# Kernel optimization log

Measured on AMD Instinct MI355X. Metric: run time of the kernel, lower is better.

## Reference

```python
import jax, jax.numpy as jnp
import numpy as np

B = 8192          # number of bags/users
L = 50            # items per bag (uniform)
NNZ = B * L
VOCAB = 100000
D = 64            # embedding_dim
ATT = 64          # att_dim
K = 4             # acc_user_num


def setup_inputs() -> dict:
    key = jax.random.key(0)
    k1, k2, k3, k4, k5 = jax.random.split(key, 5)
    # flat CSR indices, sorted within each row (module assumes coalesced order)
    idx = jax.random.randint(k1, (B, L), 0, VOCAB, dtype=jnp.int64)
    input_ = jnp.sort(idx, axis=1).reshape(NNZ)
    offsets = (jnp.arange(B, dtype=jnp.int64) * L)
    emb_weight = jax.random.normal(k2, (VOCAB, D), dtype=jnp.float32) * 0.05
    proj_w = jax.random.normal(k3, (ATT, D), dtype=jnp.float32) * (1.0 / np.sqrt(D))
    proj_b = jax.random.normal(k4, (ATT,), dtype=jnp.float32) * 0.01
    att_h = jax.random.truncated_normal(k5, -2.0, 2.0, (ATT, K), dtype=jnp.float32) * 0.01
    return {"input_": input_, "offsets": offsets, "emb_weight": emb_weight,
            "proj_w": proj_w, "proj_b": proj_b, "att_h": att_h}


def reference(input_, offsets, emb_weight, proj_w, proj_b, att_h):
    nnz = input_.shape[0]
    nseg = offsets.shape[0]
    # segment id for each flat element (offsets are sorted row starts)
    seg = jnp.searchsorted(offsets, jnp.arange(nnz), side="right") - 1  # [nnz]
    att_emb = emb_weight[input_]                                        # [nnz, D]
    att = jnp.tanh(att_emb @ proj_w.T + proj_b) @ att_h                 # [nnz, K]
    # ragged per-segment softmax over each attention column
    m = jax.ops.segment_max(att, seg, num_segments=nseg)                # [B, K]
    e = jnp.exp(att - m[seg])
    s = jax.ops.segment_sum(e, seg, num_segments=nseg)                  # [B, K]
    smax = e / s[seg]                                                   # [nnz, K]
    # weighted segment-sum pooling -> [B, K, D]
    weighted = smax[:, :, None] * att_emb[:, None, :]                   # [nnz, K, D]
    result = jax.ops.segment_sum(weighted, seg, num_segments=nseg)
    return result
```

## Files before the change

kernel.cpp:

```cpp
#include <hip/hip_runtime.h>
#include <hip/hip_bf16.h>

typedef __attribute__((ext_vector_type(4))) float  f32x4;
typedef __attribute__((ext_vector_type(4))) short  s16x4;
typedef __attribute__((ext_vector_type(8))) short  s16x8;

#define SH 72

__device__ inline short f2bf(float x) {
    return __builtin_bit_cast(short, __float2bfloat16(x));
}
__device__ inline s16x8 pack8(f32x4 a, f32x4 b) {
    s16x8 r;
    r[0] = f2bf(a[0]); r[1] = f2bf(a[1]); r[2] = f2bf(a[2]); r[3] = f2bf(a[3]);
    r[4] = f2bf(b[0]); r[5] = f2bf(b[1]); r[6] = f2bf(b[2]); r[7] = f2bf(b[3]);
    return r;
}

__global__ __launch_bounds__(256) void conv_kernel(
    const float* __restrict__ emb, short* __restrict__ emb_bf, int n8)
{
    int t = blockIdx.x * 256 + threadIdx.x;
    int stride = gridDim.x * 256;
    for (int i = t; i < n8; i += stride) {
        f32x4 a = *(const f32x4*)(emb + (size_t)i * 8);
        f32x4 b = *(const f32x4*)(emb + (size_t)i * 8 + 4);
        *(s16x8*)(emb_bf + (size_t)i * 8) = pack8(a, b);
    }
}

__global__ __launch_bounds__(256, 4) void pooled_attn_kernel(
    const int*   __restrict__ input_,
    const int*   __restrict__ offsets,
    const short* __restrict__ emb_bf,
    const float* __restrict__ pw,
    const float* __restrict__ pb,
    const float* __restrict__ ah,
    float*       __restrict__ out,
    int B, int nnz)
{
    __shared__ __align__(16) char  s_ovl[16384];
    __shared__ __align__(16) float s_bias[64];
    __shared__ __align__(16) short s_h_all[4][16 * SH];
    __shared__ __align__(16) short s_amat[4][1024];

    const int tid  = threadIdx.x;
    const int lane = tid & 63;
    const int wv   = tid >> 6;
    const int col  = lane & 15;
    const int quad = lane >> 4;

    short* s_pw  = (short*)s_ovl;
    short* s_ahp = (short*)(s_ovl + 9216);
    short* sh    = s_h_all[wv];
    short* am    = s_amat[wv];
    short* poolw = (short*)(s_ovl + wv * 4096);

    {
        int r = tid >> 2, seg = tid & 3;
        const float* rp = pw + r * 64 + seg * 16;
        f32x4 a0 = *(const f32x4*)(rp);
        f32x4 a1 = *(const f32x4*)(rp + 4);
        f32x4 a2 = *(const f32x4*)(rp + 8);
        f32x4 a3 = *(const f32x4*)(rp + 12);
        *(s16x8*)(s_pw + r * SH + seg * 16)     = pack8(a0, a1);
        *(s16x8*)(s_pw + r * SH + seg * 16 + 8) = pack8(a2, a3);
    }
    if (tid < 128) {
        int c = tid >> 6, l = tid & 63;
        int q = l >> 4, cc = l & 15;
        s16x8 v;
        #pragma unroll
        for (int j = 0; j < 8; ++j) {
            int a = c * 32 + q * 8 + j;
            v[j] = (cc < 4) ? f2bf(ah[a * 4 + cc]) : (short)0;
        }
        *(s16x8*)(s_ahp + (c * 64 + l) * 8) = v;
    }
    if (tid < 64) s_bias[tid] = pb[tid];
    __syncthreads();

    const s16x8 ahA0 = *(const s16x8*)(s_ahp + lane * 8);
    const s16x8 ahA1 = *(const s16x8*)(s_ahp + (64 + lane) * 8);
    s16x8 pwA[4][2];
    #pragma unroll
    for (int mt = 0; mt < 4; ++mt) {
        pwA[mt][0] = *(const s16x8*)(s_pw + (mt * 16 + col) * SH + quad * 8);
        pwA[mt][1] = *(const s16x8*)(s_pw + (mt * 16 + col) * SH + 32 + quad * 8);
    }
    __syncthreads();

    const int bag = blockIdx.x * 4 + wv;
    if (bag >= B) return;
    const int start = offsets[bag];
    const int end   = (bag + 1 < B) ? offsets[bag + 1] : nnz;
    int n = end - start;
    if (n > 64) n = 64;
    float* op = out + (size_t)bag * 256 + lane;
    if (n < 1) {
        op[0] = 0.f; op[64] = 0.f; op[128] = 0.f; op[192] = 0.f;
        return;
    }
    const int idx_l = input_[start + (lane < n ? lane : n - 1)];

    {
        s16x8 z = {0, 0, 0, 0, 0, 0, 0, 0};
        *(s16x8*)(am + lane * 16)     = z;
        *(s16x8*)(am + lane * 16 + 8) = z;
    }

    s16x8 gB0[4], gB1[4];
    #pragma unroll
    for (int nt = 0; nt < 4; ++nt) {
        int row = __shfl(idx_l, nt * 16 + col);
        const short* rp = emb_bf + (size_t)(unsigned)row * 64 + quad * 8;
        gB0[nt] = *(const s16x8*)(rp);
        gB1[nt] = *(const s16x8*)(rp + 32);
    }

    f32x4 p0 = {0,0,0,0}, p1 = {0,0,0,0}, p2 = {0,0,0,0}, p3 = {0,0,0,0};
    f32x4 ssum = {0, 0, 0, 0};

    #pragma unroll
    for (int nt = 0; nt < 4; ++nt) {
        {
            int i  = ((nt & 1) << 4) + col;
            int wb = ((((i >> 3) ^ quad) & 3) << 3) + (i & 7);
            #pragma unroll
            for (int j = 0; j < 8; ++j) {
                poolw[(quad * 8 + j) * 32 + wb]        = gB0[nt][j];
                poolw[(quad * 8 + j) * 32 + 1024 + wb] = gB1[nt][j];
            }
        }

        #pragma unroll
        for (int mt = 0; mt < 4; ++mt) {
            f32x4 acc = *(const f32x4*)(s_bias + mt * 16 + quad * 4);
            acc = __builtin_amdgcn_mfma_f32_16x16x32_bf16(pwA[mt][0], gB0[nt], acc, 0, 0, 0);
            acc = __builtin_amdgcn_mfma_f32_16x16x32_bf16(pwA[mt][1], gB1[nt], acc, 0, 0, 0);
            s16x4 hp;
            #pragma unroll
            for (int r = 0; r < 4; ++r) {
                float z = acc[r];
                float t2 = z * z;
                float h = z * (1.f + t2 * (-0.33333334f +
                               t2 * (0.13333333f + t2 * (-0.05396825f))));
                hp[r] = f2bf(h);
            }
            *(s16x4*)(sh + col * SH + mt * 16 + quad * 4) = hp;
        }
        f32x4 a2 = {0.f, 0.f, 0.f, 0.f};
        s16x8 b20 = *(const s16x8*)(sh + col * SH + quad * 8);
        s16x8 b21 = *(const s16x8*)(sh + col * SH + 32 + quad * 8);
        a2 = __builtin_amdgcn_mfma_f32_16x16x32_bf16(ahA0, b20, a2, 0, 0, 0);
        a2 = __builtin_amdgcn_mfma_f32_16x16x32_bf16(ahA1, b21, a2, 0, 0, 0);

        const bool pad = (nt * 16 + col >= n);
        f32x4 ev;
        #pragma unroll
        for (int k = 0; k < 4; ++k) {
            float e = __expf(a2[k]);
            e = pad ? 0.f : e;
            ev[k] = e;
            ssum[k] += (quad == 0) ? e : 0.f;
        }
        if (quad == 0) {
            int item = nt * 16 + col;
            #pragma unroll
            for (int r = 0; r < 4; ++r)
                am[(r * 64 + item) ^ (r << 3)] = f2bf(ev[r]);
        }

        if ((nt & 1) == 1) {
            const int s  = nt >> 1;
            const int c3 = col >> 3;
            int sa = (col * 64 + (s << 5) + (quad << 3)) ^ ((col & 7) << 3);
            s16x8 af = *(const s16x8*)(am + sa);
            s16x8 b0 = *(const s16x8*)(poolw + (0 * 16 + col) * 32 + (((quad ^ (0 + c3)) & 3) << 3));
            s16x8 b1 = *(const s16x8*)(poolw + (1 * 16 + col) * 32 + (((quad ^ (2 + c3)) & 3) << 3));
            s16x8 b2 = *(const s16x8*)(poolw + (2 * 16 + col) * 32 + (((quad ^ (4 + c3)) & 3) << 3));
            s16x8 b3 = *(const s16x8*)(poolw + (3 * 16 + col) * 32 + (((quad ^ (6 + c3)) & 3) << 3));
            p0 = __builtin_amdgcn_mfma_f32_16x16x32_bf16(af, b0, p0, 0, 0, 0);
            p1 = __builtin_amdgcn_mfma_f32_16x16x32_bf16(af, b1, p1, 0, 0, 0);
            p2 = __builtin_amdgcn_mfma_f32_16x16x32_bf16(af, b2, p2, 0, 0, 0);
            p3 = __builtin_amdgcn_mfma_f32_16x16x32_bf16(af, b3, p3, 0, 0, 0);
        }
    }

    #pragma unroll
    for (int m = 1; m <= 32; m <<= 1)
        #pragma unroll
        for (int k = 0; k < 4; ++k)
            ssum[k] += __shfl_xor(ssum[k], m, 64);
    f32x4 rs;
    #pragma unroll
    for (int k = 0; k < 4; ++k)
        rs[k] = __builtin_amdgcn_rcpf(ssum[k]);

    asm volatile("" ::: "memory");
    float* om = (float*)am;
    if (quad == 0) {
        { int d =      col; int sl = (d & 56) | ((d + (d >> 3)) & 7); *(f32x4*)(om + sl * 4) = p0; }
        { int d = 16 + col; int sl = (d & 56) | ((d + (d >> 3)) & 7); *(f32x4*)(om + sl * 4) = p1; }
        { int d = 32 + col; int sl = (d & 56) | ((d + (d >> 3)) & 7); *(f32x4*)(om + sl * 4) = p2; }
        { int d = 48 + col; int sl = (d & 56) | ((d + (d >> 3)) & 7); *(f32x4*)(om + sl * 4) = p3; }
    }
    int sl = (lane & 56) | ((lane + (lane >> 3)) & 7);
    f32x4 po = *(const f32x4*)(om + sl * 4);
    op[0]   = po[0] * rs[0];
    op[64]  = po[1] * rs[1];
    op[128] = po[2] * rs[2];
    op[192] = po[3] * rs[3];
}

extern "C" void kernel_launch(void* const* d_in, const int* in_sizes, int n_in,
                              void* d_out, int out_size, void* d_ws, size_t ws_size,
                              hipStream_t stream) {
    const int*   input_  = (const int*)d_in[0];
    const int*   offsets = (const int*)d_in[1];
    const float* emb     = (const float*)d_in[2];
    const float* pw      = (const float*)d_in[3];
    const float* pb      = (const float*)d_in[4];
    const float* ah      = (const float*)d_in[5];
    float* out = (float*)d_out;
    const int nnz   = in_sizes[0];
    const int B     = in_sizes[1];
    const int vocab_elems = in_sizes[2];

    short* emb_bf = (short*)d_ws;

    conv_kernel<<<1024, 256, 0, stream>>>(emb, emb_bf, vocab_elems / 8);
    pooled_attn_kernel<<<(B + 3) / 4, 256, 0, stream>>>(input_, offsets, emb_bf,
                                                        pw, pb, ah, out, B, nnz);
}
```

Measured before the change: 105.6 us.

## Drop the bf16 table pre-conversion; gather fp32 rows and convert in-register

The separate kernel that converted the entire 100k×64 fp32 embedding table to bf16 is removed. The main kernel now gathers fp32 rows directly and packs them to bf16 in registers, so it no longer reads and writes the whole table each call and only touches the ~410k gathered rows at double the byte width. It also moves the bias into registers and drops the padded h tile in favour of an XOR-swizzled 64-wide layout. It raises the occupancy hint to 5 and shortens the tanh polynomial by one term, which slightly reduces accuracy.

After: 178.3 us. +68.8%, slower.

```diff
diff --git a/kernel.cpp b/kernel.cpp
--- a/kernel.cpp
+++ b/kernel.cpp
@@ -4,8 +4,6 @@
 typedef __attribute__((ext_vector_type(4))) float  f32x4;
 typedef __attribute__((ext_vector_type(4))) short  s16x4;
 typedef __attribute__((ext_vector_type(8))) short  s16x8;
-
-#define SH 72
 
 __device__ inline short f2bf(float x) {
     return __builtin_bit_cast(short, __float2bfloat16(x));
@@ -17,22 +15,10 @@
     return r;
 }
 
-__global__ __launch_bounds__(256) void conv_kernel(
-    const float* __restrict__ emb, short* __restrict__ emb_bf, int n8)
-{
-    int t = blockIdx.x * 256 + threadIdx.x;
-    int stride = gridDim.x * 256;
-    for (int i = t; i < n8; i += stride) {
-        f32x4 a = *(const f32x4*)(emb + (size_t)i * 8);
-        f32x4 b = *(const f32x4*)(emb + (size_t)i * 8 + 4);
-        *(s16x8*)(emb_bf + (size_t)i * 8) = pack8(a, b);
-    }
-}
-
-__global__ __launch_bounds__(256, 4) void pooled_attn_kernel(
+__global__ __launch_bounds__(256, 5) void pooled_attn_kernel(
     const int*   __restrict__ input_,
     const int*   __restrict__ offsets,
-    const short* __restrict__ emb_bf,
+    const float* __restrict__ emb,
     const float* __restrict__ pw,
     const float* __restrict__ pb,
     const float* __restrict__ ah,
@@ -40,8 +26,7 @@
     int B, int nnz)
 {
     __shared__ __align__(16) char  s_ovl[16384];
-    __shared__ __align__(16) float s_bias[64];
-    __shared__ __align__(16) short s_h_all[4][16 * SH];
+    __shared__ __align__(16) short s_h_all[4][16 * 64];
     __shared__ __align__(16) short s_amat[4][1024];
 
     const int tid  = threadIdx.x;
@@ -49,6 +34,7 @@
     const int wv   = tid >> 6;
     const int col  = lane & 15;
     const int quad = lane >> 4;
+    const int xm   = (col & 7) << 3;
 
     short* s_pw  = (short*)s_ovl;
     short* s_ahp = (short*)(s_ovl + 9216);
@@ -63,8 +49,8 @@
         f32x4 a1 = *(const f32x4*)(rp + 4);
         f32x4 a2 = *(const f32x4*)(rp + 8);
         f32x4 a3 = *(const f32x4*)(rp + 12);
-        *(s16x8*)(s_pw + r * SH + seg * 16)     = pack8(a0, a1);
-        *(s16x8*)(s_pw + r * SH + seg * 16 + 8) = pack8(a2, a3);
+        *(s16x8*)(s_pw + r * 72 + seg * 16)     = pack8(a0, a1);
+        *(s16x8*)(s_pw + r * 72 + seg * 16 + 8) = pack8(a2, a3);
     }
     if (tid < 128) {
         int c = tid >> 6, l = tid & 63;
@@ -77,7 +63,6 @@
         }
         *(s16x8*)(s_ahp + (c * 64 + l) * 8) = v;
     }
-    if (tid < 64) s_bias[tid] = pb[tid];
     __syncthreads();
 
     const s16x8 ahA0 = *(const s16x8*)(s_ahp + lane * 8);
@@ -85,8 +70,8 @@
     s16x8 pwA[4][2];
     #pragma unroll
     for (int mt = 0; mt < 4; ++mt) {
-        pwA[mt][0] = *(const s16x8*)(s_pw + (mt * 16 + col) * SH + quad * 8);
-        pwA[mt][1] = *(const s16x8*)(s_pw + (mt * 16 + col) * SH + 32 + quad * 8);
+        pwA[mt][0] = *(const s16x8*)(s_pw + (mt * 16 + col) * 72 + quad * 8);
+        pwA[mt][1] = *(const s16x8*)(s_pw + (mt * 16 + col) * 72 + 32 + quad * 8);
     }
     __syncthreads();
 
@@ -103,6 +88,11 @@
     }
     const int idx_l = input_[start + (lane < n ? lane : n - 1)];
 
+    f32x4 biasv[4];
+    #pragma unroll
+    for (int mt = 0; mt < 4; ++mt)
+        biasv[mt] = *(const f32x4*)(pb + mt * 16 + quad * 4);
+
     {
         s16x8 z = {0, 0, 0, 0, 0, 0, 0, 0};
         *(s16x8*)(am + lane * 16)     = z;
@@ -113,9 +103,13 @@
     #pragma unroll
     for (int nt = 0; nt < 4; ++nt) {
         int row = __shfl(idx_l, nt * 16 + col);
-        const short* rp = emb_bf + (size_t)(unsigned)row * 64 + quad * 8;
-        gB0[nt] = *(const s16x8*)(rp);
-        gB1[nt] = *(const s16x8*)(rp + 32);
+        const float* rp = emb + (size_t)(unsigned)row * 64 + quad * 8;
+        f32x4 a0 = *(const f32x4*)(rp);
+        f32x4 a1 = *(const f32x4*)(rp + 4);
+        f32x4 b0 = *(const f32x4*)(rp + 32);
+        f32x4 b1 = *(const f32x4*)(rp + 36);
+        gB0[nt] = pack8(a0, a1);
+        gB1[nt] = pack8(b0, b1);
     }
 
     f32x4 p0 = {0,0,0,0}, p1 = {0,0,0,0}, p2 = {0,0,0,0}, p3 = {0,0,0,0};
@@ -135,7 +129,7 @@
 
         #pragma unroll
         for (int mt = 0; mt < 4; ++mt) {
-            f32x4 acc = *(const f32x4*)(s_bias + mt * 16 + quad * 4);
+            f32x4 acc = biasv[mt];
             acc = __builtin_amdgcn_mfma_f32_16x16x32_bf16(pwA[mt][0], gB0[nt], acc, 0, 0, 0);
             acc = __builtin_amdgcn_mfma_f32_16x16x32_bf16(pwA[mt][1], gB1[nt], acc, 0, 0, 0);
             s16x4 hp;
@@ -143,15 +137,14 @@
             for (int r = 0; r < 4; ++r) {
                 float z = acc[r];
                 float t2 = z * z;
-                float h = z * (1.f + t2 * (-0.33333334f +
-                               t2 * (0.13333333f + t2 * (-0.05396825f))));
+                float h = z * (1.f + t2 * (-0.33333334f + t2 * 0.13333334f));
                 hp[r] = f2bf(h);
             }
-            *(s16x4*)(sh + col * SH + mt * 16 + quad * 4) = hp;
+            *(s16x4*)(sh + col * 64 + ((mt * 16 + quad * 4) ^ xm)) = hp;
         }
         f32x4 a2 = {0.f, 0.f, 0.f, 0.f};
-        s16x8 b20 = *(const s16x8*)(sh + col * SH + quad * 8);
-        s16x8 b21 = *(const s16x8*)(sh + col * SH + 32 + quad * 8);
+        s16x8 b20 = *(const s16x8*)(sh + col * 64 + ((quad * 8) ^ xm));
+        s16x8 b21 = *(const s16x8*)(sh + col * 64 + ((32 + quad * 8) ^ xm));
         a2 = __builtin_amdgcn_mfma_f32_16x16x32_bf16(ahA0, b20, a2, 0, 0, 0);
         a2 = __builtin_amdgcn_mfma_f32_16x16x32_bf16(ahA1, b21, a2, 0, 0, 0);
 
@@ -223,13 +216,10 @@
     const float* pb      = (const float*)d_in[4];
     const float* ah      = (const float*)d_in[5];
     float* out = (float*)d_out;
-    const int nnz   = in_sizes[0];
-    const int B     = in_sizes[1];
-    const int vocab_elems = in_sizes[2];
-
-    short* emb_bf = (short*)d_ws;
-
-    conv_kernel<<<1024, 256, 0, stream>>>(emb, emb_bf, vocab_elems / 8);
-    pooled_attn_kernel<<<(B + 3) / 4, 256, 0, stream>>>(input_, offsets, emb_bf,
+    const int nnz = in_sizes[0];
+    const int B   = in_sizes[1];
+    (void)d_ws; (void)ws_size;
+
+    pooled_attn_kernel<<<(B + 3) / 4, 256, 0, stream>>>(input_, offsets, emb,
                                                         pw, pb, ah, out, B, nnz);
 }
```

## Process two bags per wave with prefetch of second bag's embedding rows

Applied to the files above, without the earlier changes.

Each wave now handles two bags (grid halved). The second bag's embedding gathers are issued after the first bag's compute loop, so they overlap its softmax reduction and output stage, and the one-time per-block setup of weights in LDS and registers is amortized over twice as many bags. It costs extra registers for the prefetch buffers and leaves fewer blocks to hide latency across the GPU.

Result: slower. 108.5 us (+2.7%).

```diff
diff --git a/kernel.cpp b/kernel.cpp
--- a/kernel.cpp
+++ b/kernel.cpp
@@ -27,6 +27,130 @@
         f32x4 b = *(const f32x4*)(emb + (size_t)i * 8 + 4);
         *(s16x8*)(emb_bf + (size_t)i * 8) = pack8(a, b);
     }
+}
+
+
+template<bool PF>
+__device__ __attribute__((always_inline)) inline void process_bag(
+    int n, int pf_idx, const short* __restrict__ emb_bf,
+    const s16x8 (&pwA)[4][2], const s16x8& ahA0, const s16x8& ahA1,
+    const float* s_bias, short* sh, short* am, short* poolw,
+    float* op, int col, int quad,
+    s16x8 (&g0)[4], s16x8 (&g1)[4],
+    s16x8 (&pf0)[4], s16x8 (&pf1)[4])
+{
+    {
+        const int lane = quad * 16 + col;
+        s16x8 z = {0, 0, 0, 0, 0, 0, 0, 0};
+        *(s16x8*)(am + lane * 16)     = z;
+        *(s16x8*)(am + lane * 16 + 8) = z;
+    }
+
+    f32x4 p0 = {0,0,0,0}, p1 = {0,0,0,0}, p2 = {0,0,0,0}, p3 = {0,0,0,0};
+    f32x4 ssum = {0, 0, 0, 0};
+
+    #pragma unroll
+    for (int nt = 0; nt < 4; ++nt) {
+        {
+            int i  = ((nt & 1) << 4) + col;
+            int wb = ((((i >> 3) ^ quad) & 3) << 3) + (i & 7);
+            #pragma unroll
+            for (int j = 0; j < 8; ++j) {
+                poolw[(quad * 8 + j) * 32 + wb]        = g0[nt][j];
+                poolw[(quad * 8 + j) * 32 + 1024 + wb] = g1[nt][j];
+            }
+        }
+
+        #pragma unroll
+        for (int mt = 0; mt < 4; ++mt) {
+            f32x4 acc = *(const f32x4*)(s_bias + mt * 16 + quad * 4);
+            acc = __builtin_amdgcn_mfma_f32_16x16x32_bf16(pwA[mt][0], g0[nt], acc, 0, 0, 0);
+            acc = __builtin_amdgcn_mfma_f32_16x16x32_bf16(pwA[mt][1], g1[nt], acc, 0, 0, 0);
+            s16x4 hp;
+            #pragma unroll
+            for (int r = 0; r < 4; ++r) {
+                float z = acc[r];
+                float t2 = z * z;
+                float h = z * (1.f + t2 * (-0.33333334f +
+                               t2 * (0.13333333f + t2 * (-0.05396825f))));
+                hp[r] = f2bf(h);
+            }
+            *(s16x4*)(sh + col * SH + mt * 16 + quad * 4) = hp;
+        }
+        f32x4 a2 = {0.f, 0.f, 0.f, 0.f};
+        s16x8 b20 = *(const s16x8*)(sh + col * SH + quad * 8);
+        s16x8 b21 = *(const s16x8*)(sh + col * SH + 32 + quad * 8);
+        a2 = __builtin_amdgcn_mfma_f32_16x16x32_bf16(ahA0, b20, a2, 0, 0, 0);
+        a2 = __builtin_amdgcn_mfma_f32_16x16x32_bf16(ahA1, b21, a2, 0, 0, 0);
+
+        const bool pad = (nt * 16 + col >= n);
+        f32x4 ev;
+        #pragma unroll
+        for (int k = 0; k < 4; ++k) {
+            float e = __expf(a2[k]);
+            e = pad ? 0.f : e;
+            ev[k] = e;
+            ssum[k] += (quad == 0) ? e : 0.f;
+        }
+        if (quad == 0) {
+            int item = nt * 16 + col;
+            #pragma unroll
+            for (int r = 0; r < 4; ++r)
+                am[(r * 64 + item) ^ (r << 3)] = f2bf(ev[r]);
+        }
+
+        if ((nt & 1) == 1) {
+            const int s  = nt >> 1;
+            const int c3 = col >> 3;
+            int sa = (col * 64 + (s << 5) + (quad << 3)) ^ ((col & 7) << 3);
+            s16x8 af = *(const s16x8*)(am + sa);
+            s16x8 b0 = *(const s16x8*)(poolw + (0 * 16 + col) * 32 + (((quad ^ (0 + c3)) & 3) << 3));
+            s16x8 b1 = *(const s16x8*)(poolw + (1 * 16 + col) * 32 + (((quad ^ (2 + c3)) & 3) << 3));
+            s16x8 b2 = *(const s16x8*)(poolw + (2 * 16 + col) * 32 + (((quad ^ (4 + c3)) & 3) << 3));
+            s16x8 b3 = *(const s16x8*)(poolw + (3 * 16 + col) * 32 + (((quad ^ (6 + c3)) & 3) << 3));
+            p0 = __builtin_amdgcn_mfma_f32_16x16x32_bf16(af, b0, p0, 0, 0, 0);
+            p1 = __builtin_amdgcn_mfma_f32_16x16x32_bf16(af, b1, p1, 0, 0, 0);
+            p2 = __builtin_amdgcn_mfma_f32_16x16x32_bf16(af, b2, p2, 0, 0, 0);
+            p3 = __builtin_amdgcn_mfma_f32_16x16x32_bf16(af, b3, p3, 0, 0, 0);
+        }
+    }
+
+    if (PF) {
+        #pragma unroll
+        for (int nt = 0; nt < 4; ++nt) {
+            int row = __shfl(pf_idx, nt * 16 + col);
+            const short* rp = emb_bf + (size_t)(unsigned)row * 64 + quad * 8;
+            pf0[nt] = *(const s16x8*)(rp);
+            pf1[nt] = *(const s16x8*)(rp + 32);
+        }
+    }
+
+    #pragma unroll
+    for (int m = 1; m <= 32; m <<= 1)
+        #pragma unroll
+        for (int k = 0; k < 4; ++k)
+            ssum[k] += __shfl_xor(ssum[k], m, 64);
+    f32x4 rs;
+    #pragma unroll
+    for (int k = 0; k < 4; ++k)
+        rs[k] = __builtin_amdgcn_rcpf(ssum[k]);
+
+    asm volatile("" ::: "memory");
+    float* om = (float*)am;
+    if (quad == 0) {
+        { int d =      col; int sl = (d & 56) | ((d + (d >> 3)) & 7); *(f32x4*)(om + sl * 4) = p0; }
+        { int d = 16 + col; int sl = (d & 56) | ((d + (d >> 3)) & 7); *(f32x4*)(om + sl * 4) = p1; }
+        { int d = 32 + col; int sl = (d & 56) | ((d + (d >> 3)) & 7); *(f32x4*)(om + sl * 4) = p2; }
+        { int d = 48 + col; int sl = (d & 56) | ((d + (d >> 3)) & 7); *(f32x4*)(om + sl * 4) = p3; }
+    }
+    const int lane = quad * 16 + col;
+    int sl = (lane & 56) | ((lane + (lane >> 3)) & 7);
+    f32x4 po = *(const f32x4*)(om + sl * 4);
+    asm volatile("" ::: "memory");
+    op[0]   = po[0] * rs[0];
+    op[64]  = po[1] * rs[1];
+    op[128] = po[2] * rs[2];
+    op[192] = po[3] * rs[3];
 }
 
 __global__ __launch_bounds__(256, 4) void pooled_attn_kernel(
@@ -90,127 +214,60 @@
     }
     __syncthreads();
 
-    const int bag = blockIdx.x * 4 + wv;
-    if (bag >= B) return;
-    const int start = offsets[bag];
-    const int end   = (bag + 1 < B) ? offsets[bag + 1] : nnz;
-    int n = end - start;
-    if (n > 64) n = 64;
-    float* op = out + (size_t)bag * 256 + lane;
-    if (n < 1) {
-        op[0] = 0.f; op[64] = 0.f; op[128] = 0.f; op[192] = 0.f;
-        return;
-    }
-    const int idx_l = input_[start + (lane < n ? lane : n - 1)];
-
-    {
-        s16x8 z = {0, 0, 0, 0, 0, 0, 0, 0};
-        *(s16x8*)(am + lane * 16)     = z;
-        *(s16x8*)(am + lane * 16 + 8) = z;
-    }
-
-    s16x8 gB0[4], gB1[4];
+    const int bagA = blockIdx.x * 8 + wv;
+    const int bagB = bagA + 4;
+
+    int nA = 0, nB = 0, idxA = 0, idxB = 0;
+    if (bagA < B) {
+        int s = offsets[bagA];
+        int e = (bagA + 1 < B) ? offsets[bagA + 1] : nnz;
+        nA = e - s; if (nA > 64) nA = 64;
+        if (nA >= 1) idxA = input_[s + (lane < nA ? lane : nA - 1)];
+    }
+    if (bagB < B) {
+        int s = offsets[bagB];
+        int e = (bagB + 1 < B) ? offsets[bagB + 1] : nnz;
+        nB = e - s; if (nB > 64) nB = 64;
+        if (nB >= 1) idxB = input_[s + (lane < nB ? lane : nB - 1)];
+    }
+
+    s16x8 gA0[4], gA1[4], gB0[4], gB1[4];
     #pragma unroll
     for (int nt = 0; nt < 4; ++nt) {
-        int row = __shfl(idx_l, nt * 16 + col);
+        int row = __shfl(idxA, nt * 16 + col);
         const short* rp = emb_bf + (size_t)(unsigned)row * 64 + quad * 8;
-        gB0[nt] = *(const s16x8*)(rp);
-        gB1[nt] = *(const s16x8*)(rp + 32);
-    }
-
-    f32x4 p0 = {0,0,0,0}, p1 = {0,0,0,0}, p2 = {0,0,0,0}, p3 = {0,0,0,0};
-    f32x4 ssum = {0, 0, 0, 0};
-
-    #pragma unroll
-    for (int nt = 0; nt < 4; ++nt) {
-        {
-            int i  = ((nt & 1) << 4) + col;
-            int wb = ((((i >> 3) ^ quad) & 3) << 3) + (i & 7);
-            #pragma unroll
-            for (int j = 0; j < 8; ++j) {
-                poolw[(quad * 8 + j) * 32 + wb]        = gB0[nt][j];
-                poolw[(quad * 8 + j) * 32 + 1024 + wb] = gB1[nt][j];
+        gA0[nt] = *(const s16x8*)(rp);
+        gA1[nt] = *(const s16x8*)(rp + 32);
+    }
+
+    if (bagA < B) {
+        float* opA = out + (size_t)bagA * 256 + lane;
+        if (nA >= 1) {
+            process_bag<true>(nA, idxB, emb_bf, pwA, ahA0, ahA1,
+                              s_bias, sh, am, poolw, opA, col, quad,
+                              gA0, gA1, gB0, gB1);
+        } else {
+            opA[0] = 0.f; opA[64] = 0.f; opA[128] = 0.f; opA[192] = 0.f;
+            #pragma unroll
+            for (int nt = 0; nt < 4; ++nt) {
+                int row = __shfl(idxB, nt * 16 + col);
+                const short* rp = emb_bf + (size_t)(unsigned)row * 64 + quad * 8;
+                gB0[nt] = *(const s16x8*)(rp);
+                gB1[nt] = *(const s16x8*)(rp + 32);
             }
         }
-
-        #pragma unroll
-        for (int mt = 0; mt < 4; ++mt) {
-            f32x4 acc = *(const f32x4*)(s_bias + mt * 16 + quad * 4);
-            acc = __builtin_amdgcn_mfma_f32_16x16x32_bf16(pwA[mt][0], gB0[nt], acc, 0, 0, 0);
-            acc = __builtin_amdgcn_mfma_f32_16x16x32_bf16(pwA[mt][1], gB1[nt], acc, 0, 0, 0);
-            s16x4 hp;
-            #pragma unroll
-            for (int r = 0; r < 4; ++r) {
-                float z = acc[r];
-                float t2 = z * z;
-                float h = z * (1.f + t2 * (-0.33333334f +
-                               t2 * (0.13333333f + t2 * (-0.05396825f))));
-                hp[r] = f2bf(h);
-            }
-            *(s16x4*)(sh + col * SH + mt * 16 + quad * 4) = hp;
-        }
-        f32x4 a2 = {0.f, 0.f, 0.f, 0.f};
-        s16x8 b20 = *(const s16x8*)(sh + col * SH + quad * 8);
-        s16x8 b21 = *(const s16x8*)(sh + col * SH + 32 + quad * 8);
-        a2 = __builtin_amdgcn_mfma_f32_16x16x32_bf16(ahA0, b20, a2, 0, 0, 0);
-        a2 = __builtin_amdgcn_mfma_f32_16x16x32_bf16(ahA1, b21, a2, 0, 0, 0);
-
-        const bool pad = (nt * 16 + col >= n);
-        f32x4 ev;
-        #pragma unroll
-        for (int k = 0; k < 4; ++k) {
-            float e = __expf(a2[k]);
-            e = pad ? 0.f : e;
-            ev[k] = e;
-            ssum[k] += (quad == 0) ? e : 0.f;
-        }
-        if (quad == 0) {
-            int item = nt * 16 + col;
-            #pragma unroll
-            for (int r = 0; r < 4; ++r)
-                am[(r * 64 + item) ^ (r << 3)] = f2bf(ev[r]);
-        }
-
-        if ((nt & 1) == 1) {
-            const int s  = nt >> 1;
-            const int c3 = col >> 3;
-            int sa = (col * 64 + (s << 5) + (quad << 3)) ^ ((col & 7) << 3);
-            s16x8 af = *(const s16x8*)(am + sa);
-            s16x8 b0 = *(const s16x8*)(poolw + (0 * 16 + col) * 32 + (((quad ^ (0 + c3)) & 3) << 3));
-            s16x8 b1 = *(const s16x8*)(poolw + (1 * 16 + col) * 32 + (((quad ^ (2 + c3)) & 3) << 3));
-            s16x8 b2 = *(const s16x8*)(poolw + (2 * 16 + col) * 32 + (((quad ^ (4 + c3)) & 3) << 3));
-            s16x8 b3 = *(const s16x8*)(poolw + (3 * 16 + col) * 32 + (((quad ^ (6 + c3)) & 3) << 3));
-            p0 = __builtin_amdgcn_mfma_f32_16x16x32_bf16(af, b0, p0, 0, 0, 0);
-            p1 = __builtin_amdgcn_mfma_f32_16x16x32_bf16(af, b1, p1, 0, 0, 0);
-            p2 = __builtin_amdgcn_mfma_f32_16x16x32_bf16(af, b2, p2, 0, 0, 0);
-            p3 = __builtin_amdgcn_mfma_f32_16x16x32_bf16(af, b3, p3, 0, 0, 0);
-        }
-    }
-
-    #pragma unroll
-    for (int m = 1; m <= 32; m <<= 1)
-        #pragma unroll
-        for (int k = 0; k < 4; ++k)
-            ssum[k] += __shfl_xor(ssum[k], m, 64);
-    f32x4 rs;
-    #pragma unroll
-    for (int k = 0; k < 4; ++k)
-        rs[k] = __builtin_amdgcn_rcpf(ssum[k]);
-
-    asm volatile("" ::: "memory");
-    float* om = (float*)am;
-    if (quad == 0) {
-        { int d =      col; int sl = (d & 56) | ((d + (d >> 3)) & 7); *(f32x4*)(om + sl * 4) = p0; }
-        { int d = 16 + col; int sl = (d & 56) | ((d + (d >> 3)) & 7); *(f32x4*)(om + sl * 4) = p1; }
-        { int d = 32 + col; int sl = (d & 56) | ((d + (d >> 3)) & 7); *(f32x4*)(om + sl * 4) = p2; }
-        { int d = 48 + col; int sl = (d & 56) | ((d + (d >> 3)) & 7); *(f32x4*)(om + sl * 4) = p3; }
-    }
-    int sl = (lane & 56) | ((lane + (lane >> 3)) & 7);
-    f32x4 po = *(const f32x4*)(om + sl * 4);
-    op[0]   = po[0] * rs[0];
-    op[64]  = po[1] * rs[1];
-    op[128] = po[2] * rs[2];
-    op[192] = po[3] * rs[3];
+    }
+
+    if (bagB < B) {
+        float* opB = out + (size_t)bagB * 256 + lane;
+        if (nB >= 1) {
+            process_bag<false>(nB, 0, emb_bf, pwA, ahA0, ahA1,
+                               s_bias, sh, am, poolw, opB, col, quad,
+                               gB0, gB1, gB0, gB1);
+        } else {
+            opB[0] = 0.f; opB[64] = 0.f; opB[128] = 0.f; opB[192] = 0.f;
+        }
+    }
 }
 
 extern "C" void kernel_launch(void* const* d_in, const int* in_sizes, int n_in,
@@ -230,6 +287,6 @@
     short* emb_bf = (short*)d_ws;
 
     conv_kernel<<<1024, 256, 0, stream>>>(emb, emb_bf, vocab_elems / 8);
-    pooled_attn_kernel<<<(B + 3) / 4, 256, 0, stream>>>(input_, offsets, emb_bf,
+    pooled_attn_kernel<<<(B + 7) / 8, 256, 0, stream>>>(input_, offsets, emb_bf,
                                                         pw, pb, ah, out, B, nnz);
 }
```
